# Kernel tuning notes

Measured on AMD Instinct MI355X. Metric: run time of the kernel, lower is better.

## Reference

```python
import jax, jax.numpy as jnp
import numpy as np

H, W = 96, 96
THRESHOLD = 0.9
C = 256

def setup_inputs() -> dict:
    key = jax.random.key(0)
    k1, k2 = jax.random.split(key)
    return {
        "feature_query": jax.random.normal(k1, (C, H, W), jnp.float32),
        "feature_projection": jax.random.normal(k2, (C, H, W), jnp.float32),
    }

def reference(feature_query, feature_projection):
    c = feature_query.shape[0]
    # flatten spatial dims -> [C, N]; L2-normalize each pixel's descriptor over channels
    q = feature_query.reshape(c, -1)
    p = feature_projection.reshape(c, -1)
    q = q / jnp.linalg.norm(q, axis=0, keepdims=True)
    p = p / jnp.linalg.norm(p, axis=0, keepdims=True)
    # cosine similarity matrix [N, M] (GEMM)
    sim = jnp.einsum('cn,cm->nm', q, p)
    col_max = jnp.argmax(sim, axis=0)   # [M] best query row per projection column
    row_max = jnp.argmax(sim, axis=1)   # [N] best projection column per query row
    j = jnp.arange(sim.shape[1])
    q_idx = col_max                      # candidate query index for each column j
    sim_vals = sim[q_idx, j]
    # mutual nearest-neighbor + threshold (fixed-shape boolean mask instead of
    # a data-dependent python list, for jit compatibility)
    mutual = (row_max[q_idx] == j) & (sim_vals > THRESHOLD)
    # oneDim2TwoDim: (idx // W, idx % W), valid only if div+1 < H
    q_div, q_mod = q_idx // W, q_idx % W
    p_div, p_mod = j // W, j % W
    valid = mutual & (q_div + 1 < H) & (p_div + 1 < H)
    return sim, valid, q_idx, q_div, q_mod, p_div, p_mod
```

## Files before the change

kernel.cpp:

```cpp
#include <hip/hip_runtime.h>
#include <hip/hip_fp16.h>

#define N_PIX 9216
#define CCH 256
#define W_ 96
#define H_ 96
#define BM 128
#define BN 128
#define BK 16
#define TM 8
#define TN 8

typedef _Float16 half8_t __attribute__((ext_vector_type(8)));
typedef float f32x4_t __attribute__((ext_vector_type(4)));

__device__ __forceinline__ unsigned int mono_enc(float f) {
    unsigned int u = __float_as_uint(f);
    return (u & 0x80000000u) ? ~u : (u | 0x80000000u);
}
__device__ __forceinline__ float mono_dec(unsigned int e) {
    return __uint_as_float((e & 0x80000000u) ? (e ^ 0x80000000u) : ~e);
}


__global__ __launch_bounds__(256) void norms_kernel(const float* __restrict__ Q,
                                                    const float* __restrict__ P,
                                                    float* __restrict__ invq,
                                                    float* __restrict__ invp) {
    int n = blockIdx.x * blockDim.x + threadIdx.x;
    if (n >= N_PIX) return;
    float sq = 0.f, sp = 0.f;
    for (int c = 0; c < CCH; ++c) {
        float a = Q[(size_t)c * N_PIX + n];
        float b = P[(size_t)c * N_PIX + n];
        sq = fmaf(a, a, sq);
        sp = fmaf(b, b, sp);
    }
    invq[n] = 1.0f / sqrtf(sq);
    invp[n] = 1.0f / sqrtf(sp);
}

__device__ __forceinline__ int local_row(int ty, int i) {
    return (i < 4) ? (ty * 4 + i) : (64 + ty * 4 + (i - 4));
}
__device__ __forceinline__ int local_col(int tx, int j) {
    return (j < 4) ? (tx * 4 + j) : (64 + tx * 4 + (j - 4));
}

__global__ __launch_bounds__(256) void gemm_kernel(const float* __restrict__ Q,
                                                   const float* __restrict__ P,
                                                   const float* __restrict__ invq,
                                                   const float* __restrict__ invp,
                                                   float* __restrict__ sim,
                                                   unsigned long long* __restrict__ row_best,
                                                   unsigned long long* __restrict__ col_best) {
    __shared__ union SH {
        struct { float A[BK][BM]; float B[BK][BN]; } t;
        unsigned long long red[16][128];
    } sh;

    const int tid = threadIdx.x;
    const int tx = tid & 15;
    const int ty = tid >> 4;
    const int n0 = blockIdx.y * BM;
    const int m0 = blockIdx.x * BN;

    float acc[TM][TN];
#pragma unroll
    for (int i = 0; i < TM; ++i)
#pragma unroll
        for (int j = 0; j < TN; ++j) acc[i][j] = 0.f;

    for (int kk = 0; kk < CCH; kk += BK) {
#pragma unroll
        for (int rep = 0; rep < 2; ++rep) {
            int idx = tid + rep * 256;
            int row = idx >> 5;
            int c4  = idx & 31;
            float4 av = *(const float4*)&Q[(size_t)(kk + row) * N_PIX + n0 + c4 * 4];
            float4 bv = *(const float4*)&P[(size_t)(kk + row) * N_PIX + m0 + c4 * 4];
            *(float4*)&sh.t.A[row][c4 * 4] = av;
            *(float4*)&sh.t.B[row][c4 * 4] = bv;
        }
        __syncthreads();
#pragma unroll
        for (int k = 0; k < BK; ++k) {
            float a[TM], b[TN];
            *(float4*)&a[0] = *(const float4*)&sh.t.A[k][ty * 4];
            *(float4*)&a[4] = *(const float4*)&sh.t.A[k][ty * 4 + 64];
            *(float4*)&b[0] = *(const float4*)&sh.t.B[k][tx * 4];
            *(float4*)&b[4] = *(const float4*)&sh.t.B[k][tx * 4 + 64];
#pragma unroll
            for (int i = 0; i < TM; ++i)
#pragma unroll
                for (int j = 0; j < TN; ++j)
                    acc[i][j] = fmaf(a[i], b[j], acc[i][j]);
        }
        __syncthreads();
    }

    float iq[TM], ip[TN];
#pragma unroll
    for (int i = 0; i < TM; ++i) iq[i] = invq[n0 + local_row(ty, i)];
#pragma unroll
    for (int j = 0; j < TN; ++j) ip[j] = invp[m0 + local_col(tx, j)];
#pragma unroll
    for (int i = 0; i < TM; ++i)
#pragma unroll
        for (int j = 0; j < TN; ++j) acc[i][j] *= iq[i] * ip[j];

#pragma unroll
    for (int i = 0; i < TM; ++i) {
        int n = n0 + local_row(ty, i);
        float4 v0 = make_float4(acc[i][0], acc[i][1], acc[i][2], acc[i][3]);
        float4 v1 = make_float4(acc[i][4], acc[i][5], acc[i][6], acc[i][7]);
        float* dst = &sim[(size_t)n * N_PIX + m0];
        *(float4*)(dst + tx * 4) = v0;
        *(float4*)(dst + 64 + tx * 4) = v1;
    }

#pragma unroll
    for (int i = 0; i < TM; ++i) {
        float best = acc[i][0]; int bj = 0;
#pragma unroll
        for (int j = 1; j < TN; ++j)
            if (acc[i][j] > best) { best = acc[i][j]; bj = j; }
        unsigned int gcol = (unsigned int)(m0 + local_col(tx, bj));
        sh.red[tx][local_row(ty, i)] =
            ((unsigned long long)mono_enc(best) << 32) | (unsigned long long)(0xFFFFFFFFu - gcol);
    }
    __syncthreads();
    if (tid < 128) {
        unsigned long long best = sh.red[0][tid];
#pragma unroll
        for (int x = 1; x < 16; ++x) {
            unsigned long long v = sh.red[x][tid];
            if (v > best) best = v;
        }
        atomicMax(&row_best[n0 + tid], best);
    }
    __syncthreads();

#pragma unroll
    for (int j = 0; j < TN; ++j) {
        float best = acc[0][j]; int bi = 0;
#pragma unroll
        for (int i = 1; i < TM; ++i)
            if (acc[i][j] > best) { best = acc[i][j]; bi = i; }
        unsigned int grow = (unsigned int)(n0 + local_row(ty, bi));
        sh.red[ty][local_col(tx, j)] =
            ((unsigned long long)mono_enc(best) << 32) | (unsigned long long)(0xFFFFFFFFu - grow);
    }
    __syncthreads();
    if (tid < 128) {
        unsigned long long best = sh.red[0][tid];
#pragma unroll
        for (int x = 1; x < 16; ++x) {
            unsigned long long v = sh.red[x][tid];
            if (v > best) best = v;
        }
        atomicMax(&col_best[m0 + tid], best);
    }
}


__global__ __launch_bounds__(256) void norms4_kernel(const float* __restrict__ Q,
                                                     const float* __restrict__ P,
                                                     float* __restrict__ invq,
                                                     float* __restrict__ invp) {
    __shared__ float rq[4][64];
    __shared__ float rp[4][64];
    const int lane = threadIdx.x & 63;
    const int band = threadIdx.x >> 6;
    const int n = blockIdx.x * 64 + lane;
    float sq = 0.f, sp = 0.f;
    for (int k = band * 64; k < (band + 1) * 64; ++k) {
        float a = Q[(size_t)k * N_PIX + n];
        float b = P[(size_t)k * N_PIX + n];
        sq = fmaf(a, a, sq);
        sp = fmaf(b, b, sp);
    }
    rq[band][lane] = sq;
    rp[band][lane] = sp;
    __syncthreads();
    if (threadIdx.x < 64) {
        float tq = rq[0][lane] + rq[1][lane] + rq[2][lane] + rq[3][lane];
        float tp = rp[0][lane] + rp[1][lane] + rp[2][lane] + rp[3][lane];
        invq[n] = 1.0f / sqrtf(tq);
        invp[n] = 1.0f / sqrtf(tp);
    }
}

__global__ __launch_bounds__(256) void split_kernel(const float* __restrict__ Q,
                                                    const float* __restrict__ P,
                                                    unsigned int* __restrict__ qh,
                                                    unsigned int* __restrict__ ql,
                                                    unsigned int* __restrict__ ph,
                                                    unsigned int* __restrict__ pl) {
    const int n = blockIdx.x * 256 + threadIdx.x;
    const int k2 = blockIdx.y;
    const size_t i0 = (size_t)(2 * k2) * N_PIX + n;
    const size_t o  = (size_t)k2 * N_PIX + n;

    float a0 = Q[i0], a1 = Q[i0 + N_PIX];
    unsigned short qh0 = __half_as_ushort(__float2half(a0));
    unsigned short qh1 = __half_as_ushort(__float2half(a1));
    float qr0 = a0 - __half2float(__ushort_as_half(qh0));
    float qr1 = a1 - __half2float(__ushort_as_half(qh1));
    unsigned short ql0 = __half_as_ushort(__float2half(qr0));
    unsigned short ql1 = __half_as_ushort(__float2half(qr1));
    qh[o] = (unsigned int)qh0 | ((unsigned int)qh1 << 16);
    ql[o] = (unsigned int)ql0 | ((unsigned int)ql1 << 16);

    float b0 = P[i0], b1 = P[i0 + N_PIX];
    unsigned short ph0 = __half_as_ushort(__float2half(b0));
    unsigned short ph1 = __half_as_ushort(__float2half(b1));
    float pr0 = b0 - __half2float(__ushort_as_half(ph0));
    float pr1 = b1 - __half2float(__ushort_as_half(ph1));
    unsigned short pl0 = __half_as_ushort(__float2half(pr0));
    unsigned short pl1 = __half_as_ushort(__float2half(pr1));
    ph[o] = (unsigned int)ph0 | ((unsigned int)ph1 << 16);
    pl[o] = (unsigned int)pl0 | ((unsigned int)pl1 << 16);
}

__global__ __launch_bounds__(256, 2) void mfma_gemm_kernel(
        const unsigned int* __restrict__ QH, const unsigned int* __restrict__ QL,
        const unsigned int* __restrict__ PH, const unsigned int* __restrict__ PL,
        const float* __restrict__ invq, const float* __restrict__ invp,
        float* __restrict__ sim,
        unsigned long long* __restrict__ row_best,
        unsigned long long* __restrict__ col_best) {
    const unsigned int bid = blockIdx.x;
    const unsigned int nb = (bid & 7u) * 648u + (bid >> 3);
    const unsigned int by = nb / 72u;
    const unsigned int bx = nb % 72u;

    const int tid = threadIdx.x;
    const int l  = tid & 63;
    const int w  = tid >> 6;
    const int rl = l & 15;
    const int kg = l >> 4;
    const int r0 = (int)by * 128 + (w >> 1) * 64;
    const int c0 = (int)bx * 128 + (w & 1) * 64;

    const f32x4_t zero4 = {0.f, 0.f, 0.f, 0.f};
    f32x4_t acc[4][4];
#pragma unroll
    for (int i = 0; i < 4; ++i)
#pragma unroll
        for (int j = 0; j < 4; ++j) acc[i][j] = zero4;

    const unsigned int rA = (unsigned int)(r0 + rl);
    const unsigned int cB = (unsigned int)(c0 + rl);

    union Frag { unsigned int u[4]; half8_t h; };

    for (int kd0 = 0; kd0 < 128; kd0 += 16) {
        const int kd = kd0 + kg * 4;
        Frag ah[4], al[4], bh[4], bl[4];
#pragma unroll
        for (int j = 0; j < 4; ++j) {
            const unsigned int* qhp = QH + (size_t)(kd + j) * N_PIX + rA;
            const unsigned int* qlp = QL + (size_t)(kd + j) * N_PIX + rA;
            const unsigned int* php = PH + (size_t)(kd + j) * N_PIX + cB;
            const unsigned int* plp = PL + (size_t)(kd + j) * N_PIX + cB;
#pragma unroll
            for (int f = 0; f < 4; ++f) {
                ah[f].u[j] = qhp[f * 16];
                al[f].u[j] = qlp[f * 16];
                bh[f].u[j] = php[f * 16];
                bl[f].u[j] = plp[f * 16];
            }
        }
#pragma unroll
        for (int fr = 0; fr < 4; ++fr)
#pragma unroll
            for (int fc = 0; fc < 4; ++fc) {
                acc[fr][fc] = __builtin_amdgcn_mfma_f32_16x16x32_f16(ah[fr].h, bh[fc].h, acc[fr][fc], 0, 0, 0);
                acc[fr][fc] = __builtin_amdgcn_mfma_f32_16x16x32_f16(ah[fr].h, bl[fc].h, acc[fr][fc], 0, 0, 0);
                acc[fr][fc] = __builtin_amdgcn_mfma_f32_16x16x32_f16(al[fr].h, bh[fc].h, acc[fr][fc], 0, 0, 0);
            }
    }

    float iq[4][4];
#pragma unroll
    for (int fr = 0; fr < 4; ++fr) {
        const float4 v = *(const float4*)&invq[r0 + fr * 16 + kg * 4];
        iq[fr][0] = v.x; iq[fr][1] = v.y; iq[fr][2] = v.z; iq[fr][3] = v.w;
    }
    float ip[4];
#pragma unroll
    for (int fc = 0; fc < 4; ++fc) ip[fc] = invp[c0 + fc * 16 + rl];

#pragma unroll
    for (int fr = 0; fr < 4; ++fr)
#pragma unroll
        for (int j = 0; j < 4; ++j) {
            const int r = r0 + fr * 16 + kg * 4 + j;
            float* dst = sim + (size_t)r * N_PIX;
#pragma unroll
            for (int fc = 0; fc < 4; ++fc) {
                float v = acc[fr][fc][j] * iq[fr][j] * ip[fc];
                acc[fr][fc][j] = v;
                __builtin_nontemporal_store(v, dst + c0 + fc * 16 + rl);
            }
        }

#pragma unroll
    for (int fr = 0; fr < 4; ++fr)
#pragma unroll
        for (int j = 0; j < 4; ++j) {
            float best = acc[fr][0][j];
            int bf = 0;
#pragma unroll
            for (int fc = 1; fc < 4; ++fc)
                if (acc[fr][fc][j] > best) { best = acc[fr][fc][j]; bf = fc; }
            const unsigned int gcol = (unsigned int)(c0 + bf * 16 + rl);
            unsigned long long key = ((unsigned long long)mono_enc(best) << 32)
                                   | (unsigned long long)(0xFFFFFFFFu - gcol);
#pragma unroll
            for (int m = 1; m < 16; m <<= 1) {
                unsigned long long o = __shfl_xor(key, m, 64);
                if (o > key) key = o;
            }
            if (rl == 0)
                atomicMax(&row_best[r0 + fr * 16 + kg * 4 + j], key);
        }

#pragma unroll
    for (int fc = 0; fc < 4; ++fc) {
        float best = acc[0][fc][0];
        unsigned int brow = (unsigned int)(r0 + kg * 4);
#pragma unroll
        for (int fr = 0; fr < 4; ++fr)
#pragma unroll
            for (int j = 0; j < 4; ++j) {
                float v = acc[fr][fc][j];
                unsigned int rr = (unsigned int)(r0 + fr * 16 + kg * 4 + j);
                if (v > best) { best = v; brow = rr; }
            }
        unsigned long long key = ((unsigned long long)mono_enc(best) << 32)
                               | (unsigned long long)(0xFFFFFFFFu - brow);
#pragma unroll
        for (int m = 16; m < 64; m <<= 1) {
            unsigned long long o = __shfl_xor(key, m, 64);
            if (o > key) key = o;
        }
        if (kg == 0)
            atomicMax(&col_best[c0 + fc * 16 + rl], key);
    }
}


__global__ __launch_bounds__(256) void epilogue_kernel(const unsigned long long* __restrict__ row_best,
                                                       const unsigned long long* __restrict__ col_best,
                                                       float* __restrict__ out) {
    int j = blockIdx.x * blockDim.x + threadIdx.x;
    if (j >= N_PIX) return;
    unsigned long long cb = col_best[j];
    unsigned int q_idx = 0xFFFFFFFFu - (unsigned int)(cb & 0xFFFFFFFFull);
    float simval = mono_dec((unsigned int)(cb >> 32));
    unsigned long long rb = row_best[q_idx];
    unsigned int rm = 0xFFFFFFFFu - (unsigned int)(rb & 0xFFFFFFFFull);
    bool mutual = (rm == (unsigned int)j) && (simval > 0.9f);
    int qd = (int)(q_idx / W_), qm = (int)(q_idx % W_);
    int pd = j / W_, pm = j % W_;
    bool valid = mutual && (qd + 1 < H_) && (pd + 1 < H_);
    size_t base = (size_t)N_PIX * N_PIX;
    out[base + 0 * (size_t)N_PIX + j] = valid ? 1.0f : 0.0f;
    out[base + 1 * (size_t)N_PIX + j] = (float)q_idx;
    out[base + 2 * (size_t)N_PIX + j] = (float)qd;
    out[base + 3 * (size_t)N_PIX + j] = (float)qm;
    out[base + 4 * (size_t)N_PIX + j] = (float)pd;
    out[base + 5 * (size_t)N_PIX + j] = (float)pm;
}

extern "C" void kernel_launch(void* const* d_in, const int* in_sizes, int n_in,
                              void* d_out, int out_size, void* d_ws, size_t ws_size,
                              hipStream_t stream) {
    const float* Q = (const float*)d_in[0];
    const float* P = (const float*)d_in[1];
    float* out = (float*)d_out;

    unsigned long long* row_best = (unsigned long long*)d_ws;
    unsigned long long* col_best = row_best + N_PIX;
    float* invq = (float*)(col_best + N_PIX);
    float* invp = invq + N_PIX;

    hipMemsetAsync(d_ws, 0, 2 * N_PIX * sizeof(unsigned long long), stream);

    const size_t base_bytes = 2 * N_PIX * sizeof(unsigned long long) + 2 * N_PIX * sizeof(float);
    const size_t arr_dwords = (size_t)(CCH / 2) * N_PIX;
    const size_t need = base_bytes + 4 * arr_dwords * sizeof(unsigned int);

    if (ws_size >= need) {
        unsigned int* qh = (unsigned int*)((char*)d_ws + base_bytes);
        unsigned int* ql = qh + arr_dwords;
        unsigned int* ph = ql + arr_dwords;
        unsigned int* pl = ph + arr_dwords;

        norms4_kernel<<<N_PIX / 64, 256, 0, stream>>>(Q, P, invq, invp);
        split_kernel<<<dim3(N_PIX / 256, CCH / 2), 256, 0, stream>>>(Q, P, qh, ql, ph, pl);
        mfma_gemm_kernel<<<5184, 256, 0, stream>>>(qh, ql, ph, pl, invq, invp,
                                                   out, row_best, col_best);
    } else {
        norms_kernel<<<N_PIX / 256, 256, 0, stream>>>(Q, P, invq, invp);
        dim3 grid(N_PIX / BN, N_PIX / BM);
        gemm_kernel<<<grid, 256, 0, stream>>>(Q, P, invq, invp, out, row_best, col_best);
    }

    epilogue_kernel<<<N_PIX / 256, 256, 0, stream>>>(row_best, col_best, out);
}
```

Before: 541.1 us.

## Fuse norm and fp16 split prep, repack operands as uint4, stage sim stores through LDS

Merges the norm and hi/lo fp16 split kernels into one prep kernel that writes operands in an 8-channel uint4-packed layout. The GEMM can then load each MFMA fragment with a single 16-byte load instead of four dword loads. The block-to-tile mapping is reworked for XCD/L2 locality and the occupancy hint is raised to 3. The sim output is transposed through shared memory so it is written as coalesced 16-byte nontemporal stores. This adds LDS use and register pressure, which the higher launch bound may turn into spills.

```diff
diff --git a/kernel.cpp b/kernel.cpp
--- a/kernel.cpp
+++ b/kernel.cpp
@@ -164,21 +164,56 @@
 }
 
 
-__global__ __launch_bounds__(256) void norms4_kernel(const float* __restrict__ Q,
-                                                     const float* __restrict__ P,
-                                                     float* __restrict__ invq,
-                                                     float* __restrict__ invp) {
+__device__ __forceinline__ unsigned int pack_pair(float x, float y, float& rx, float& ry) {
+    __half hx = __float2half(x), hy = __float2half(y);
+    rx = x - __half2float(hx);
+    ry = y - __half2float(hy);
+    return (unsigned int)__half_as_ushort(hx) | ((unsigned int)__half_as_ushort(hy) << 16);
+}
+
+__global__ __launch_bounds__(256) void prep_kernel(const float* __restrict__ Q,
+                                                   const float* __restrict__ P,
+                                                   uint4* __restrict__ qh,
+                                                   uint4* __restrict__ ql,
+                                                   uint4* __restrict__ ph,
+                                                   uint4* __restrict__ pl,
+                                                   float* __restrict__ invq,
+                                                   float* __restrict__ invp) {
     __shared__ float rq[4][64];
     __shared__ float rp[4][64];
     const int lane = threadIdx.x & 63;
     const int band = threadIdx.x >> 6;
     const int n = blockIdx.x * 64 + lane;
     float sq = 0.f, sp = 0.f;
-    for (int k = band * 64; k < (band + 1) * 64; ++k) {
-        float a = Q[(size_t)k * N_PIX + n];
-        float b = P[(size_t)k * N_PIX + n];
-        sq = fmaf(a, a, sq);
-        sp = fmaf(b, b, sp);
+    for (int kb = band * 8; kb < band * 8 + 8; ++kb) {
+        float a[8], b[8];
+#pragma unroll
+        for (int t = 0; t < 8; ++t) {
+            a[t] = Q[(size_t)(kb * 8 + t) * N_PIX + n];
+            b[t] = P[(size_t)(kb * 8 + t) * N_PIX + n];
+        }
+#pragma unroll
+        for (int t = 0; t < 8; ++t) {
+            sq = fmaf(a[t], a[t], sq);
+            sp = fmaf(b[t], b[t], sp);
+        }
+        uint4 vqh, vql, vph, vpl;
+        unsigned int* uqh = (unsigned int*)&vqh;
+        unsigned int* uql = (unsigned int*)&vql;
+        unsigned int* uph = (unsigned int*)&vph;
+        unsigned int* upl = (unsigned int*)&vpl;
+#pragma unroll
+        for (int j = 0; j < 4; ++j) {
+            float r0, r1;
+            uqh[j] = pack_pair(a[2 * j], a[2 * j + 1], r0, r1);
+            uql[j] = (unsigned int)__half_as_ushort(__float2half(r0))
+                   | ((unsigned int)__half_as_ushort(__float2half(r1)) << 16);
+            uph[j] = pack_pair(b[2 * j], b[2 * j + 1], r0, r1);
+            upl[j] = (unsigned int)__half_as_ushort(__float2half(r0))
+                   | ((unsigned int)__half_as_ushort(__float2half(r1)) << 16);
+        }
+        size_t o = (size_t)kb * N_PIX + n;
+        qh[o] = vqh; ql[o] = vql; ph[o] = vph; pl[o] = vpl;
     }
     rq[band][lane] = sq;
     rp[band][lane] = sp;
@@ -191,49 +226,20 @@
     }
 }
 
-__global__ __launch_bounds__(256) void split_kernel(const float* __restrict__ Q,
-                                                    const float* __restrict__ P,
-                                                    unsigned int* __restrict__ qh,
-                                                    unsigned int* __restrict__ ql,
-                                                    unsigned int* __restrict__ ph,
-                                                    unsigned int* __restrict__ pl) {
-    const int n = blockIdx.x * 256 + threadIdx.x;
-    const int k2 = blockIdx.y;
-    const size_t i0 = (size_t)(2 * k2) * N_PIX + n;
-    const size_t o  = (size_t)k2 * N_PIX + n;
-
-    float a0 = Q[i0], a1 = Q[i0 + N_PIX];
-    unsigned short qh0 = __half_as_ushort(__float2half(a0));
-    unsigned short qh1 = __half_as_ushort(__float2half(a1));
-    float qr0 = a0 - __half2float(__ushort_as_half(qh0));
-    float qr1 = a1 - __half2float(__ushort_as_half(qh1));
-    unsigned short ql0 = __half_as_ushort(__float2half(qr0));
-    unsigned short ql1 = __half_as_ushort(__float2half(qr1));
-    qh[o] = (unsigned int)qh0 | ((unsigned int)qh1 << 16);
-    ql[o] = (unsigned int)ql0 | ((unsigned int)ql1 << 16);
-
-    float b0 = P[i0], b1 = P[i0 + N_PIX];
-    unsigned short ph0 = __half_as_ushort(__float2half(b0));
-    unsigned short ph1 = __half_as_ushort(__float2half(b1));
-    float pr0 = b0 - __half2float(__ushort_as_half(ph0));
-    float pr1 = b1 - __half2float(__ushort_as_half(ph1));
-    unsigned short pl0 = __half_as_ushort(__float2half(pr0));
-    unsigned short pl1 = __half_as_ushort(__float2half(pr1));
-    ph[o] = (unsigned int)ph0 | ((unsigned int)ph1 << 16);
-    pl[o] = (unsigned int)pl0 | ((unsigned int)pl1 << 16);
-}
-
-__global__ __launch_bounds__(256, 2) void mfma_gemm_kernel(
-        const unsigned int* __restrict__ QH, const unsigned int* __restrict__ QL,
-        const unsigned int* __restrict__ PH, const unsigned int* __restrict__ PL,
+__global__ __launch_bounds__(256, 3) void mfma_gemm_kernel(
+        const uint4* __restrict__ QH, const uint4* __restrict__ QL,
+        const uint4* __restrict__ PH, const uint4* __restrict__ PL,
         const float* __restrict__ invq, const float* __restrict__ invp,
         float* __restrict__ sim,
         unsigned long long* __restrict__ row_best,
         unsigned long long* __restrict__ col_best) {
     const unsigned int bid = blockIdx.x;
-    const unsigned int nb = (bid & 7u) * 648u + (bid >> 3);
-    const unsigned int by = nb / 72u;
-    const unsigned int bx = nb % 72u;
+    const unsigned int xcd = bid & 7u;
+    const unsigned int nbl = bid >> 3;
+    const unsigned int gg  = nbl / 72u;
+    const unsigned int rr  = nbl % 72u;
+    const unsigned int by  = xcd * 9u + (rr >> 3);
+    const unsigned int bx  = gg * 8u + (rr & 7u);
 
     const int tid = threadIdx.x;
     const int l  = tid & 63;
@@ -243,6 +249,8 @@
     const int r0 = (int)by * 128 + (w >> 1) * 64;
     const int c0 = (int)bx * 128 + (w & 1) * 64;
 
+    __shared__ float st[4][16][68];
+
     const f32x4_t zero4 = {0.f, 0.f, 0.f, 0.f};
     f32x4_t acc[4][4];
 #pragma unroll
@@ -250,35 +258,32 @@
 #pragma unroll
         for (int j = 0; j < 4; ++j) acc[i][j] = zero4;
 
-    const unsigned int rA = (unsigned int)(r0 + rl);
-    const unsigned int cB = (unsigned int)(c0 + rl);
-
-    union Frag { unsigned int u[4]; half8_t h; };
-
-    for (int kd0 = 0; kd0 < 128; kd0 += 16) {
-        const int kd = kd0 + kg * 4;
-        Frag ah[4], al[4], bh[4], bl[4];
-#pragma unroll
-        for (int j = 0; j < 4; ++j) {
-            const unsigned int* qhp = QH + (size_t)(kd + j) * N_PIX + rA;
-            const unsigned int* qlp = QL + (size_t)(kd + j) * N_PIX + rA;
-            const unsigned int* php = PH + (size_t)(kd + j) * N_PIX + cB;
-            const unsigned int* plp = PL + (size_t)(kd + j) * N_PIX + cB;
-#pragma unroll
-            for (int f = 0; f < 4; ++f) {
-                ah[f].u[j] = qhp[f * 16];
-                al[f].u[j] = qlp[f * 16];
-                bh[f].u[j] = php[f * 16];
-                bl[f].u[j] = plp[f * 16];
-            }
-        }
+    const int rA = r0 + rl;
+    const int cB = c0 + rl;
+
+    const uint4* pqh = QH + (size_t)kg * N_PIX + rA;
+    const uint4* pql = QL + (size_t)kg * N_PIX + rA;
+    const uint4* pph = PH + (size_t)kg * N_PIX + cB;
+    const uint4* ppl = PL + (size_t)kg * N_PIX + cB;
+
+#pragma unroll 2
+    for (int ks = 0; ks < 8; ++ks) {
+        half8_t ah[4], al4[4], bh4[4], bl4[4];
+#pragma unroll
+        for (int f = 0; f < 4; ++f) {
+            ah[f]  = *(const half8_t*)(pqh + f * 16);
+            al4[f] = *(const half8_t*)(pql + f * 16);
+            bh4[f] = *(const half8_t*)(pph + f * 16);
+            bl4[f] = *(const half8_t*)(ppl + f * 16);
+        }
+        pqh += 4 * N_PIX; pql += 4 * N_PIX; pph += 4 * N_PIX; ppl += 4 * N_PIX;
 #pragma unroll
         for (int fr = 0; fr < 4; ++fr)
 #pragma unroll
             for (int fc = 0; fc < 4; ++fc) {
-                acc[fr][fc] = __builtin_amdgcn_mfma_f32_16x16x32_f16(ah[fr].h, bh[fc].h, acc[fr][fc], 0, 0, 0);
-                acc[fr][fc] = __builtin_amdgcn_mfma_f32_16x16x32_f16(ah[fr].h, bl[fc].h, acc[fr][fc], 0, 0, 0);
-                acc[fr][fc] = __builtin_amdgcn_mfma_f32_16x16x32_f16(al[fr].h, bh[fc].h, acc[fr][fc], 0, 0, 0);
+                acc[fr][fc] = __builtin_amdgcn_mfma_f32_16x16x32_f16(ah[fr],  bh4[fc], acc[fr][fc], 0, 0, 0);
+                acc[fr][fc] = __builtin_amdgcn_mfma_f32_16x16x32_f16(ah[fr],  bl4[fc], acc[fr][fc], 0, 0, 0);
+                acc[fr][fc] = __builtin_amdgcn_mfma_f32_16x16x32_f16(al4[fr], bh4[fc], acc[fr][fc], 0, 0, 0);
             }
     }
 
@@ -295,16 +300,10 @@
 #pragma unroll
     for (int fr = 0; fr < 4; ++fr)
 #pragma unroll
-        for (int j = 0; j < 4; ++j) {
-            const int r = r0 + fr * 16 + kg * 4 + j;
-            float* dst = sim + (size_t)r * N_PIX;
-#pragma unroll
-            for (int fc = 0; fc < 4; ++fc) {
-                float v = acc[fr][fc][j] * iq[fr][j] * ip[fc];
-                acc[fr][fc][j] = v;
-                __builtin_nontemporal_store(v, dst + c0 + fc * 16 + rl);
-            }
-        }
+        for (int fc = 0; fc < 4; ++fc)
+#pragma unroll
+            for (int j = 0; j < 4; ++j)
+                acc[fr][fc][j] *= iq[fr][j] * ip[fc];
 
 #pragma unroll
     for (int fr = 0; fr < 4; ++fr)
@@ -336,8 +335,8 @@
 #pragma unroll
             for (int j = 0; j < 4; ++j) {
                 float v = acc[fr][fc][j];
-                unsigned int rr = (unsigned int)(r0 + fr * 16 + kg * 4 + j);
-                if (v > best) { best = v; brow = rr; }
+                unsigned int rr2 = (unsigned int)(r0 + fr * 16 + kg * 4 + j);
+                if (v > best) { best = v; brow = rr2; }
             }
         unsigned long long key = ((unsigned long long)mono_enc(best) << 32)
                                | (unsigned long long)(0xFFFFFFFFu - brow);
@@ -348,6 +347,24 @@
         }
         if (kg == 0)
             atomicMax(&col_best[c0 + fc * 16 + rl], key);
+    }
+
+#pragma unroll
+    for (int fr = 0; fr < 4; ++fr) {
+        asm volatile("s_waitcnt lgkmcnt(0)" ::: "memory");
+#pragma unroll
+        for (int fc = 0; fc < 4; ++fc)
+#pragma unroll
+            for (int j = 0; j < 4; ++j)
+                st[w][kg * 4 + j][fc * 16 + rl] = acc[fr][fc][j];
+        asm volatile("s_waitcnt lgkmcnt(0)" ::: "memory");
+#pragma unroll
+        for (int pass = 0; pass < 4; ++pass) {
+            const int rowL = pass * 4 + kg;
+            const f32x4_t v = *(const f32x4_t*)&st[w][rowL][rl * 4];
+            const int gr = r0 + fr * 16 + rowL;
+            __builtin_nontemporal_store(v, (f32x4_t*)(sim + (size_t)gr * N_PIX + c0 + rl * 4));
+        }
     }
 }
 
@@ -390,17 +407,16 @@
     hipMemsetAsync(d_ws, 0, 2 * N_PIX * sizeof(unsigned long long), stream);
 
     const size_t base_bytes = 2 * N_PIX * sizeof(unsigned long long) + 2 * N_PIX * sizeof(float);
-    const size_t arr_dwords = (size_t)(CCH / 2) * N_PIX;
-    const size_t need = base_bytes + 4 * arr_dwords * sizeof(unsigned int);
+    const size_t arr_u4 = (size_t)(CCH / 8) * N_PIX;
+    const size_t need = base_bytes + 4 * arr_u4 * sizeof(uint4);
 
     if (ws_size >= need) {
-        unsigned int* qh = (unsigned int*)((char*)d_ws + base_bytes);
-        unsigned int* ql = qh + arr_dwords;
-        unsigned int* ph = ql + arr_dwords;
-        unsigned int* pl = ph + arr_dwords;
-
-        norms4_kernel<<<N_PIX / 64, 256, 0, stream>>>(Q, P, invq, invp);
-        split_kernel<<<dim3(N_PIX / 256, CCH / 2), 256, 0, stream>>>(Q, P, qh, ql, ph, pl);
+        uint4* qh = (uint4*)((char*)d_ws + base_bytes);
+        uint4* ql = qh + arr_u4;
+        uint4* ph = ql + arr_u4;
+        uint4* pl = ph + arr_u4;
+
+        prep_kernel<<<N_PIX / 64, 256, 0, stream>>>(Q, P, qh, ql, ph, pl, invq, invp);
         mfma_gemm_kernel<<<5184, 256, 0, stream>>>(qh, ql, ph, pl, invq, invp,
                                                    out, row_best, col_best);
     } else {
```

Result: faster. 485.2 us (-10.3%).
